# Kernel optimization log

Measured on AMD Instinct MI355X. Metric: run time of the kernel, lower is better.

Reference implementation:

```python
import jax, jax.numpy as jnp
import numpy as np

B, F, A, H = 131072, 32, 8, 64  # batch, n_features, n_actions, hidden

def setup_inputs() -> dict:
    key = jax.random.key(0)
    k = jax.random.split(key, 6)
    return {
        "f_t": jax.random.normal(k[0], (B, F), dtype=jnp.float32),
        "a_t": jax.random.normal(k[1], (B, A), dtype=jnp.float32),
        "W1": jax.random.normal(k[2], (F, F + A, H), dtype=jnp.float32) * 0.1,
        "b1": jax.random.normal(k[3], (F, H), dtype=jnp.float32) * 0.1,
        "W2": jax.random.normal(k[4], (F, H), dtype=jnp.float32) * 0.1,
        "b2": jax.random.normal(k[5], (F,), dtype=jnp.float32) * 0.1,
    }

def reference(f_t, a_t, W1, b1, W2, b2):
    # fa_t: [B, F+A] shared input to all F submodels
    fa_t = jnp.concatenate((f_t, a_t), axis=1)
    # Batched grouped-GEMM over the F independent submodels.
    h = jax.nn.relu(jnp.einsum('bi,fih->bfh', fa_t, W1) + b1)  # [B, F, H]
    f_t1 = jnp.einsum('bfh,fh->bf', h, W2) + b2                 # [B, F]
    # skip_connection=True
    return f_t1 + f_t
```

## Files before the change

kernel.cpp:

```cpp
#include <hip/hip_runtime.h>

#define B_TOTAL 131072
#define NF 32
#define NA 8
#define NH 64

using frag_ab = __attribute__((ext_vector_type(8))) short;
using f32x16  = __attribute__((ext_vector_type(16))) float;
typedef int   v2i __attribute__((ext_vector_type(2)));
typedef float v2f __attribute__((ext_vector_type(2)));

__device__ __forceinline__ unsigned short f2bf(float x) {
  unsigned u = __float_as_uint(x);
  u = (u + 0x7FFFu + ((u >> 16) & 1u)) >> 16;
  return (unsigned short)u;
}

__global__ void pack_w1_kernel(const float* __restrict__ W1, const float* __restrict__ b1,
                               unsigned short* __restrict__ w1p) {
  int idx = blockIdx.x * 256 + threadIdx.x;
  int j = idx & 7, l = (idx >> 3) & 63, tq = idx >> 9;
  int q = tq % 6, f = tq / 6;
  int ht = q / 3, kt = q % 3;
  int h = ht * 32 + (l & 31);
  int i = kt * 16 + ((l >> 5) << 3) + j;
  float v = 0.0f;
  if (i < NF + NA)       v = W1[(f * (NF + NA) + i) * NH + h];
  else if (i == NF + NA) v = b1[f * NH + h];
  w1p[idx] = f2bf(v);
}

__global__ void pack_w2_kernel(const float* __restrict__ W2, float* __restrict__ w2p) {
  int idx = blockIdx.x * 256 + threadIdx.x;
  int r = idx & 15, ht = (idx >> 4) & 1, g = (idx >> 5) & 1, f = idx >> 6;
  w2p[idx] = W2[f * NH + ht * 32 + (r & 3) + 8 * (r >> 2) + 4 * g];
}

__device__ __forceinline__ v2f pk_fma(v2f a, v2f b, v2f c) {
  v2f d;
  asm("v_pk_fma_f32 %0, %1, %2, %3" : "=v"(d) : "v"(a), "v"(b), "v"(c));
  return d;
}

__device__ __forceinline__ float xor32_add(float v) {
  v2i p = __builtin_amdgcn_permlane32_swap(__float_as_int(v), __float_as_int(v), false, false);
  return __int_as_float(p.x) + __int_as_float(p.y);
}

__global__ __launch_bounds__(256, 2) void fused_mlp_kernel(
    const float* __restrict__ ft, const float* __restrict__ at,
    const unsigned short* __restrict__ w1p, const float* __restrict__ w2p,
    const float* __restrict__ b2, float* __restrict__ out) {
  __shared__ __align__(16) unsigned short wlds[2][12288];

  const int t = threadIdx.x;
  const int wv = t >> 6;
  const int l = t & 63;
  const int g = l >> 5;
  const int lc = l & 31;
  const long rowb = (long)blockIdx.x * 256 + wv * 64;

  {
    const unsigned short* src = w1p + t * 8;
#pragma unroll
    for (int k = 0; k < 6; ++k)
      __builtin_amdgcn_global_load_lds((const __attribute__((address_space(1))) void*)(src + k * 2048),
                                       (__attribute__((address_space(3))) void*)(&wlds[0][k * 2048 + t * 8]), 16, 0, 0);
  }

  frag_ab bfr[2][3];
#pragma unroll
  for (int bt = 0; bt < 2; ++bt) {
    const long b = rowb + bt * 32 + lc;
    const float* fr = ft + b * NF;
    float tmp[8];
#pragma unroll
    for (int kt = 0; kt < 2; ++kt) {
      *(float4*)tmp       = *(const float4*)(fr + kt * 16 + g * 8);
      *(float4*)(tmp + 4) = *(const float4*)(fr + kt * 16 + g * 8 + 4);
      frag_ab fb;
#pragma unroll
      for (int j = 0; j < 8; ++j) fb[j] = (short)f2bf(tmp[j]);
      bfr[bt][kt] = fb;
    }
    *(float4*)tmp       = *(const float4*)(at + b * NA);
    *(float4*)(tmp + 4) = *(const float4*)(at + b * NA + 4);
    frag_ab fb;
#pragma unroll
    for (int j = 0; j < 8; ++j) {
      unsigned short bias = (j == 0) ? (unsigned short)0x3F80 : (unsigned short)0;
      fb[j] = (short)((g == 0) ? f2bf(tmp[j]) : bias);
    }
    bfr[bt][2] = fb;
  }

  const f32x16 zero16 = {0.f,0.f,0.f,0.f,0.f,0.f,0.f,0.f,0.f,0.f,0.f,0.f,0.f,0.f,0.f,0.f};
  float res[NF];

  for (int r = 0; r < 8; ++r) {
    __syncthreads();

    if (r < 7) {
      const unsigned short* src = w1p + (r + 1) * 12288 + t * 8;
#pragma unroll
      for (int k = 0; k < 6; ++k)
        __builtin_amdgcn_global_load_lds((const __attribute__((address_space(1))) void*)(src + k * 2048),
                                         (__attribute__((address_space(3))) void*)(&wlds[(r + 1) & 1][k * 2048 + t * 8]), 16, 0, 0);
    }

    const unsigned short* buf = wlds[r & 1];

#pragma unroll
    for (int fo = 0; fo < 4; ++fo) {
      const int f = r * 4 + fo;

      frag_ab wf[2][3];
#pragma unroll
      for (int ht = 0; ht < 2; ++ht)
#pragma unroll
        for (int kt = 0; kt < 3; ++kt)
          wf[ht][kt] = *(const frag_ab*)&buf[((fo * 6 + ht * 3 + kt) * 64 + l) * 8];

      float4 wq[8];
      const float4* wp = (const float4*)w2p + (f * 2 + g) * 8;
#pragma unroll
      for (int q = 0; q < 8; ++q) wq[q] = wp[q];

      float sb[2];
#pragma unroll
      for (int bt = 0; bt < 2; ++bt) {
        f32x16 a0 = zero16, a1 = zero16;
#pragma unroll
        for (int kt = 0; kt < 3; ++kt) {
          a0 = __builtin_amdgcn_mfma_f32_32x32x16_bf16(wf[0][kt], bfr[bt][kt], a0, 0, 0, 0);
          a1 = __builtin_amdgcn_mfma_f32_32x32x16_bf16(wf[1][kt], bfr[bt][kt], a1, 0, 0, 0);
        }
        v2f ps0 = {0.f, 0.f}, ps1 = {0.f, 0.f};
#pragma unroll
        for (int rq = 0; rq < 4; ++rq) {
          float4 w0 = wq[rq], w1 = wq[4 + rq];
          v2f m;
          m[0] = fmaxf(a0[rq * 4 + 0], 0.f); m[1] = fmaxf(a0[rq * 4 + 1], 0.f);
          ps0 = pk_fma(m, (v2f){w0.x, w0.y}, ps0);
          m[0] = fmaxf(a0[rq * 4 + 2], 0.f); m[1] = fmaxf(a0[rq * 4 + 3], 0.f);
          ps0 = pk_fma(m, (v2f){w0.z, w0.w}, ps0);
          m[0] = fmaxf(a1[rq * 4 + 0], 0.f); m[1] = fmaxf(a1[rq * 4 + 1], 0.f);
          ps1 = pk_fma(m, (v2f){w1.x, w1.y}, ps1);
          m[0] = fmaxf(a1[rq * 4 + 2], 0.f); m[1] = fmaxf(a1[rq * 4 + 3], 0.f);
          ps1 = pk_fma(m, (v2f){w1.z, w1.w}, ps1);
        }
        float s = (ps0[0] + ps0[1]) + (ps1[0] + ps1[1]);
        sb[bt] = xor32_add(s);
      }
      res[f] = g ? sb[1] : sb[0];
    }
  }

  const long row = rowb + l;
  const float4* fr = (const float4*)(ft + row * NF);
  const float4* bb = (const float4*)b2;
  float4* op = (float4*)(out + row * NF);
#pragma unroll
  for (int q = 0; q < 8; ++q) {
    float4 x = fr[q], bv = bb[q], o;
    o.x = res[q * 4 + 0] + bv.x + x.x;
    o.y = res[q * 4 + 1] + bv.y + x.y;
    o.z = res[q * 4 + 2] + bv.z + x.z;
    o.w = res[q * 4 + 3] + bv.w + x.w;
    op[q] = o;
  }
}

extern "C" void kernel_launch(void* const* d_in, const int* in_sizes, int n_in,
                              void* d_out, int out_size, void* d_ws, size_t ws_size,
                              hipStream_t stream) {
  const float* ft = (const float*)d_in[0];
  const float* at = (const float*)d_in[1];
  const float* W1 = (const float*)d_in[2];
  const float* b1 = (const float*)d_in[3];
  const float* W2 = (const float*)d_in[4];
  const float* b2 = (const float*)d_in[5];
  float* out = (float*)d_out;

  unsigned short* w1p = (unsigned short*)d_ws;
  float* w2p = (float*)((char*)d_ws + (1u << 18));

  pack_w1_kernel<<<384, 256, 0, stream>>>(W1, b1, w1p);
  pack_w2_kernel<<<16, 256, 0, stream>>>(W2, w2p);
  fused_mlp_kernel<<<B_TOTAL / 256, 256, 0, stream>>>(ft, at, w1p, w2p, b2, out);
}
```

Baseline: 61.41 us.

## Halve rows per wave and weight staging to raise occupancy

Each wave processes 32 batch rows instead of 64, features are staged two per round over sixteen rounds, and LDS is halved so four blocks can fit per CU. The grid doubles in size. The aim is more latency hiding through occupancy and lower register pressure. In exchange, weight fragments are reloaded from LDS per 32 rows instead of per 64, there are more barriers per row, and the output epilogue indexes the result array by lane half, which may force scratch usage.

```diff
diff --git a/kernel.cpp b/kernel.cpp
--- a/kernel.cpp
+++ b/kernel.cpp
@@ -47,31 +47,30 @@
   return __int_as_float(p.x) + __int_as_float(p.y);
 }
 
-__global__ __launch_bounds__(256, 2) void fused_mlp_kernel(
+__global__ __launch_bounds__(256, 4) void fused_mlp_kernel(
     const float* __restrict__ ft, const float* __restrict__ at,
     const unsigned short* __restrict__ w1p, const float* __restrict__ w2p,
     const float* __restrict__ b2, float* __restrict__ out) {
-  __shared__ __align__(16) unsigned short wlds[2][12288];
+  __shared__ __align__(16) unsigned short wlds[2][6144];
 
   const int t = threadIdx.x;
   const int wv = t >> 6;
   const int l = t & 63;
   const int g = l >> 5;
   const int lc = l & 31;
-  const long rowb = (long)blockIdx.x * 256 + wv * 64;
+  const long rowb = (long)blockIdx.x * 128 + wv * 32;
 
   {
     const unsigned short* src = w1p + t * 8;
 #pragma unroll
-    for (int k = 0; k < 6; ++k)
+    for (int k = 0; k < 3; ++k)
       __builtin_amdgcn_global_load_lds((const __attribute__((address_space(1))) void*)(src + k * 2048),
                                        (__attribute__((address_space(3))) void*)(&wlds[0][k * 2048 + t * 8]), 16, 0, 0);
   }
 
-  frag_ab bfr[2][3];
-#pragma unroll
-  for (int bt = 0; bt < 2; ++bt) {
-    const long b = rowb + bt * 32 + lc;
+  frag_ab bfr[3];
+  {
+    const long b = rowb + lc;
     const float* fr = ft + b * NF;
     float tmp[8];
 #pragma unroll
@@ -81,7 +80,7 @@
       frag_ab fb;
 #pragma unroll
       for (int j = 0; j < 8; ++j) fb[j] = (short)f2bf(tmp[j]);
-      bfr[bt][kt] = fb;
+      bfr[kt] = fb;
     }
     *(float4*)tmp       = *(const float4*)(at + b * NA);
     *(float4*)(tmp + 4) = *(const float4*)(at + b * NA + 4);
@@ -91,19 +90,19 @@
       unsigned short bias = (j == 0) ? (unsigned short)0x3F80 : (unsigned short)0;
       fb[j] = (short)((g == 0) ? f2bf(tmp[j]) : bias);
     }
-    bfr[bt][2] = fb;
+    bfr[2] = fb;
   }
 
   const f32x16 zero16 = {0.f,0.f,0.f,0.f,0.f,0.f,0.f,0.f,0.f,0.f,0.f,0.f,0.f,0.f,0.f,0.f};
   float res[NF];
 
-  for (int r = 0; r < 8; ++r) {
+  for (int r = 0; r < 16; ++r) {
     __syncthreads();
 
-    if (r < 7) {
-      const unsigned short* src = w1p + (r + 1) * 12288 + t * 8;
+    if (r < 15) {
+      const unsigned short* src = w1p + (r + 1) * 6144 + t * 8;
 #pragma unroll
-      for (int k = 0; k < 6; ++k)
+      for (int k = 0; k < 3; ++k)
         __builtin_amdgcn_global_load_lds((const __attribute__((address_space(1))) void*)(src + k * 2048),
                                          (__attribute__((address_space(3))) void*)(&wlds[(r + 1) & 1][k * 2048 + t * 8]), 16, 0, 0);
     }
@@ -111,8 +110,8 @@
     const unsigned short* buf = wlds[r & 1];
 
 #pragma unroll
-    for (int fo = 0; fo < 4; ++fo) {
-      const int f = r * 4 + fo;
+    for (int fo = 0; fo < 2; ++fo) {
+      const int f = r * 2 + fo;
 
       frag_ab wf[2][3];
 #pragma unroll
@@ -126,48 +125,45 @@
 #pragma unroll
       for (int q = 0; q < 8; ++q) wq[q] = wp[q];
 
-      float sb[2];
+      f32x16 a0 = zero16, a1 = zero16;
 #pragma unroll
-      for (int bt = 0; bt < 2; ++bt) {
-        f32x16 a0 = zero16, a1 = zero16;
+      for (int kt = 0; kt < 3; ++kt) {
+        a0 = __builtin_amdgcn_mfma_f32_32x32x16_bf16(wf[0][kt], bfr[kt], a0, 0, 0, 0);
+        a1 = __builtin_amdgcn_mfma_f32_32x32x16_bf16(wf[1][kt], bfr[kt], a1, 0, 0, 0);
+      }
+      v2f ps0 = {0.f, 0.f}, ps1 = {0.f, 0.f};
 #pragma unroll
-        for (int kt = 0; kt < 3; ++kt) {
-          a0 = __builtin_amdgcn_mfma_f32_32x32x16_bf16(wf[0][kt], bfr[bt][kt], a0, 0, 0, 0);
-          a1 = __builtin_amdgcn_mfma_f32_32x32x16_bf16(wf[1][kt], bfr[bt][kt], a1, 0, 0, 0);
-        }
-        v2f ps0 = {0.f, 0.f}, ps1 = {0.f, 0.f};
-#pragma unroll
-        for (int rq = 0; rq < 4; ++rq) {
-          float4 w0 = wq[rq], w1 = wq[4 + rq];
-          v2f m;
-          m[0] = fmaxf(a0[rq * 4 + 0], 0.f); m[1] = fmaxf(a0[rq * 4 + 1], 0.f);
-          ps0 = pk_fma(m, (v2f){w0.x, w0.y}, ps0);
-          m[0] = fmaxf(a0[rq * 4 + 2], 0.f); m[1] = fmaxf(a0[rq * 4 + 3], 0.f);
-          ps0 = pk_fma(m, (v2f){w0.z, w0.w}, ps0);
-          m[0] = fmaxf(a1[rq * 4 + 0], 0.f); m[1] = fmaxf(a1[rq * 4 + 1], 0.f);
-          ps1 = pk_fma(m, (v2f){w1.x, w1.y}, ps1);
-          m[0] = fmaxf(a1[rq * 4 + 2], 0.f); m[1] = fmaxf(a1[rq * 4 + 3], 0.f);
-          ps1 = pk_fma(m, (v2f){w1.z, w1.w}, ps1);
-        }
-        float s = (ps0[0] + ps0[1]) + (ps1[0] + ps1[1]);
-        sb[bt] = xor32_add(s);
+      for (int rq = 0; rq < 4; ++rq) {
+        float4 w0 = wq[rq], w1 = wq[4 + rq];
+        v2f m;
+        m[0] = fmaxf(a0[rq * 4 + 0], 0.f); m[1] = fmaxf(a0[rq * 4 + 1], 0.f);
+        ps0 = pk_fma(m, (v2f){w0.x, w0.y}, ps0);
+        m[0] = fmaxf(a0[rq * 4 + 2], 0.f); m[1] = fmaxf(a0[rq * 4 + 3], 0.f);
+        ps0 = pk_fma(m, (v2f){w0.z, w0.w}, ps0);
+        m[0] = fmaxf(a1[rq * 4 + 0], 0.f); m[1] = fmaxf(a1[rq * 4 + 1], 0.f);
+        ps1 = pk_fma(m, (v2f){w1.x, w1.y}, ps1);
+        m[0] = fmaxf(a1[rq * 4 + 2], 0.f); m[1] = fmaxf(a1[rq * 4 + 3], 0.f);
+        ps1 = pk_fma(m, (v2f){w1.z, w1.w}, ps1);
       }
-      res[f] = g ? sb[1] : sb[0];
+      float s = (ps0[0] + ps0[1]) + (ps1[0] + ps1[1]);
+      res[f] = xor32_add(s);
     }
   }
 
-  const long row = rowb + l;
-  const float4* fr = (const float4*)(ft + row * NF);
-  const float4* bb = (const float4*)b2;
-  float4* op = (float4*)(out + row * NF);
+  const long row = rowb + lc;
+  const float* fr = ft + row * NF + g * 16;
+  const float* bb = b2 + g * 16;
+  float* op = out + row * NF + g * 16;
 #pragma unroll
-  for (int q = 0; q < 8; ++q) {
-    float4 x = fr[q], bv = bb[q], o;
-    o.x = res[q * 4 + 0] + bv.x + x.x;
-    o.y = res[q * 4 + 1] + bv.y + x.y;
-    o.z = res[q * 4 + 2] + bv.z + x.z;
-    o.w = res[q * 4 + 3] + bv.w + x.w;
-    op[q] = o;
+  for (int q = 0; q < 4; ++q) {
+    float4 x = *(const float4*)(fr + q * 4);
+    float4 bv = *(const float4*)(bb + q * 4);
+    float4 o;
+    o.x = res[g * 16 + q * 4 + 0] + bv.x + x.x;
+    o.y = res[g * 16 + q * 4 + 1] + bv.y + x.y;
+    o.z = res[g * 16 + q * 4 + 2] + bv.z + x.z;
+    o.w = res[g * 16 + q * 4 + 3] + bv.w + x.w;
+    *(float4*)(op + q * 4) = o;
   }
 }
 
@@ -187,5 +183,5 @@
 
   pack_w1_kernel<<<384, 256, 0, stream>>>(W1, b1, w1p);
   pack_w2_kernel<<<16, 256, 0, stream>>>(W2, w2p);
-  fused_mlp_kernel<<<B_TOTAL / 256, 256, 0, stream>>>(ft, at, w1p, w2p, b2, out);
+  fused_mlp_kernel<<<B_TOTAL / 128, 256, 0, stream>>>(ft, at, w1p, w2p, b2, out);
 }
```

Measured after the change: 64.73 us. 5.4% more time.
